# Optimization experiments

Hardware: AMD Instinct MI355X
Metric: run time of the kernel (lower is better)

## Reference

```python
import jax, jax.numpy as jnp
import numpy as np

B, N, E, F, U = 256, 240, 4338, 28, 100
NEG_SLOPE = 0.2  # PyG GATConv default negative_slope


def setup_inputs() -> dict:
    key = jax.random.key(0)
    ks = jax.random.split(key, 13)
    s = 0.05  # xavier-ish scale
    return {
        "inputs": jax.random.normal(ks[0], (B, N * F), jnp.float32),
        "state": jax.random.normal(ks[1], (B, N * U), jnp.float32),
        "edge_src": jax.random.randint(ks[2], (E,), 0, N, jnp.int32),
        "edge_dst": jax.random.randint(ks[3], (E,), 0, N, jnp.int32),
        # GATConv(U+F -> U): linear weight, attention vectors, output bias
        "Wg": jax.random.normal(ks[4], (U, U + F), jnp.float32) * s,
        "att_src": jax.random.normal(ks[5], (U,), jnp.float32) * s,
        "att_dst": jax.random.normal(ks[6], (U,), jnp.float32) * s,
        "gat_bias": jnp.zeros((U,), jnp.float32),
        # bias_1 added in _gc3 (self.biases[(100,)])
        "bias1": jnp.zeros((U,), jnp.float32),
        # GRU1: GRULinear(100, 200); GRU2: GRULinear(100, 100)
        "W_ru": jax.random.normal(ks[7], (U + F, 2 * U), jnp.float32) * s,
        "b_ru": jnp.zeros((2 * U,), jnp.float32),
        "W_c": jax.random.normal(ks[8], (U + F, U), jnp.float32) * s,
        "b_c": jnp.zeros((U,), jnp.float32),
    }


def _gat_gru(inputs, state, src, dst, Wg, att_src, att_dst, gat_bias, bias1,
             W_ru, b_ru, W_c, b_c):
    xi = inputs.reshape(B, N, F)
    xs = state.reshape(B, N, U)
    # _gc3: concat [state, inputs] -> GATConv per sample (vectorized here)
    x = jnp.concatenate([xs, xi], axis=2)                 # [B, N, U+F]
    h = jnp.einsum("bnf,cf->bnc", x, Wg)                  # [B, N, U]
    a_src = h @ att_src                                    # [B, N]
    a_dst = h @ att_dst                                    # [B, N]
    e = jax.nn.leaky_relu(a_src[:, src] + a_dst[:, dst], NEG_SLOPE)  # [B, E+N]
    eT = e.T                                               # [E+N, B]
    emax = jax.ops.segment_max(eT, dst, num_segments=N)    # [N, B]
    ex = jnp.exp(eT - emax[dst])
    denom = jax.ops.segment_sum(ex, dst, num_segments=N)   # [N, B]
    alpha = ex / denom[dst]                                # [E+N, B]
    msgs = h[:, src].transpose(1, 0, 2) * alpha[:, :, None]  # [E+N, B, U]
    agg = jax.ops.segment_sum(msgs, dst, num_segments=N)   # [N, B, U]
    gstate = agg.transpose(1, 0, 2) + gat_bias + bias1     # [B, N, U]
    st = gstate.reshape(B, N * U)
    # GRU gates (GRULinear concatenates [inputs, hidden] on feature dim)
    cat1 = jnp.concatenate([xi, gstate], axis=2).reshape(-1, U + F)
    ru = jax.nn.sigmoid((cat1 @ W_ru + b_ru).reshape(B, N, 2 * U))
    r = ru[..., :U].reshape(B, N * U)
    u = ru[..., U:].reshape(B, N * U)
    cat2 = jnp.concatenate([xi, (r * st).reshape(B, N, U)], axis=2).reshape(-1, U + F)
    c = jnp.tanh(cat2 @ W_c + b_c).reshape(B, N * U)
    return u * st + (1.0 - u) * c


def reference(inputs, state, edge_src, edge_dst, Wg, att_src, att_dst,
              gat_bias, bias1, W_ru, b_ru, W_c, b_c):
    # PyG GATConv default add_self_loops=True
    loops = jnp.arange(N, dtype=edge_src.dtype)
    src = jnp.concatenate([edge_src, loops])
    dst = jnp.concatenate([edge_dst, loops])
    return _gat_gru(inputs, state, src, dst, Wg, att_src, att_dst, gat_bias,
                    bias1, W_ru, b_ru, W_c, b_c)
```

## Files before the change

kernel.cpp:

```cpp
#include <hip/hip_runtime.h>

#define Bb 256
#define Nn 240
#define Ee 4338
#define Ff 28
#define Uu 100
#define Kk 128
#define AS 136
#define KP 248

typedef __attribute__((ext_vector_type(8))) short bf16x8;
typedef __attribute__((ext_vector_type(4))) float f32x4;
typedef unsigned short u16;

__device__ __forceinline__ float bf2f(u16 u) {
  union { unsigned int i; float f; } v; v.i = ((unsigned int)u) << 16; return v.f;
}
__device__ __forceinline__ u16 f2bf(float f) {
  union { float ff; unsigned int i; } v; v.ff = f;
  unsigned int x = v.i;
  return (u16)((x + 0x7fffu + ((x >> 16) & 1u)) >> 16);
}
__device__ __forceinline__ void split4(const float4 v, ushort4& h, ushort4& l) {
  u16 h0 = f2bf(v.x), h1 = f2bf(v.y), h2 = f2bf(v.z), h3 = f2bf(v.w);
  h.x = h0; h.y = h1; h.z = h2; h.w = h3;
  l.x = f2bf(v.x - bf2f(h0)); l.y = f2bf(v.y - bf2f(h1));
  l.z = f2bf(v.z - bf2f(h2)); l.w = f2bf(v.w - bf2f(h3));
}

__global__ __launch_bounds__(512, 2) void k_fused(
    const float* __restrict__ stt, const float* __restrict__ inp,
    const float* __restrict__ Wg,
    const float* __restrict__ att_s, const float* __restrict__ att_d,
    const int* __restrict__ esrc, const int* __restrict__ edst,
    const float* __restrict__ gbias, const float* __restrict__ b1,
    const float* __restrict__ Wru, const float* __restrict__ bru,
    const float* __restrict__ Wc, const float* __restrict__ bc,
    float* __restrict__ out) {
  __shared__ __align__(16) char smem[154752];
  u16*      hTH    = (u16*)(smem);
  u16*      hTL    = (u16*)(smem + 49600);
  u16*      panel  = (u16*)(smem + 99200);
  u16*      ahL    = panel;
  u16*      alL    = panel + 32 * AS;
  u16*      alphaL = panel;
  float*    gch    = (float*)(smem + 116608);
  u16*      panel2 = (u16*)(smem + 116608);
  u16*      alphaH = (u16*)(smem + 129408);
  u16*      ugQ    = (u16*)(smem + 145280);
  float*    asrcL  = (float*)(smem + 151680);
  float*    adstL  = (float*)(smem + 152640);
  float*    denC   = (float*)(smem + 153600);
  float*    w_asL  = (float*)(smem + 153728);
  float*    w_adL  = (float*)(smem + 154240);

  int tid = threadIdx.x;
  int b = blockIdx.x;
  const size_t sbase = (size_t)b * Nn * Uu;
  const size_t ibase = (size_t)b * Nn * Ff;

  int w = tid >> 6, l = tid & 63, l15 = l & 15, q = l >> 4;
  int cw = w * 16 + l15;

  f32x4 zero = {0.f, 0.f, 0.f, 0.f};
  bf16x8 z8 = {0, 0, 0, 0, 0, 0, 0, 0};

  auto stageChunk = [&](u16* buf, int c0, int rowsn, int base, int stride) {
    for (int j = base; j < rowsn * 32; j += stride) {
      int r = j >> 5, g = j & 31;
      float4 v = (g < 25)
          ? *(const float4*)(stt + sbase + (size_t)(c0 + r) * Uu + g * 4)
          : *(const float4*)(inp + ibase + (size_t)(c0 + r) * Ff + (g - 25) * 4);
      ushort4 hh, lo;
      split4(v, hh, lo);
      *(ushort4*)(buf + r * AS + g * 4) = hh;
      *(ushort4*)(buf + 32 * AS + r * AS + g * 4) = lo;
    }
  };

  auto histChunk = [&](int c0, int rowsn) {
    unsigned* cbase = (unsigned*)alphaH;
    for (int e = tid; e < Ee; e += 512) {
      int d = edst[e];
      unsigned r = (unsigned)(d - c0);
      if (r < (unsigned)rowsn) {
        int s = esrc[e];
        atomicAdd(&cbase[r * 124 + (s >> 1)], 1u << (16 * (s & 1)));
      }
    }
    if (tid < rowsn) {
      int n = c0 + tid;
      atomicAdd(&cbase[tid * 124 + (n >> 1)], 1u << (16 * (n & 1)));
    }
  };

  if (tid < 256) {
    int k = tid & 127;
    const float* av = (tid < 128) ? att_s : att_d;
    float acc = 0.f;
    for (int c = 0; c < Uu; ++c) acc += Wg[c * Kk + k] * av[c];
    ((tid < 128) ? w_asL : w_adL)[k] = acc;
  } else {
    stageChunk(panel, 0, 32, tid - 256, 256);
  }
  __syncthreads();

  {
    bf16x8 wh[4], wl[4];
#pragma unroll
    for (int s = 0; s < 4; ++s) {
#pragma unroll
      for (int j = 0; j < 8; ++j) {
        int kp = s * 32 + q * 8 + j;
        float v = (cw < Uu) ? Wg[cw * Kk + kp]
                : (cw == Uu) ? w_asL[kp]
                : (cw == Uu + 1) ? w_adL[kp] : 0.f;
        u16 hh = f2bf(v);
        wh[s][j] = (short)hh;
        wl[s][j] = (short)f2bf(v - bf2f(hh));
      }
    }

    for (int ch0 = 0; ch0 < Nn; ch0 += 32) {
      int rows = Nn - ch0; if (rows > 32) rows = 32;
      int nrt = rows >> 4;
      u16* bufc = ((ch0 >> 5) & 1) ? panel2 : panel;
      int nx = ch0 + 32;
      if (nx < Nn) {
        int rowsn = Nn - nx; if (rowsn > 32) rowsn = 32;
        stageChunk(((nx >> 5) & 1) ? panel2 : panel, nx, rowsn, tid, 512);
      }
      f32x4 acc[2]; acc[0] = zero; acc[1] = zero;
#pragma unroll
      for (int rt = 0; rt < 2; ++rt) if (rt < nrt) {
#pragma unroll
        for (int s = 0; s < 4; ++s) {
          bf16x8 a = *(const bf16x8*)(bufc + (rt * 16 + l15) * AS + s * 32 + q * 8);
          bf16x8 bb = *(const bf16x8*)(bufc + 32 * AS + (rt * 16 + l15) * AS + s * 32 + q * 8);
          acc[rt] = __builtin_amdgcn_mfma_f32_16x16x32_bf16(a, wh[s], acc[rt], 0, 0, 0);
          acc[rt] = __builtin_amdgcn_mfma_f32_16x16x32_bf16(bb, wh[s], acc[rt], 0, 0, 0);
          acc[rt] = __builtin_amdgcn_mfma_f32_16x16x32_bf16(a, wl[s], acc[rt], 0, 0, 0);
        }
      }
#pragma unroll
      for (int rt = 0; rt < 2; ++rt) if (rt < nrt) {
#pragma unroll
        for (int i = 0; i < 4; ++i) {
          float v = acc[rt][i];
          int krow = ch0 + rt * 16 + q * 4 + i;
          if (cw < Uu) {
            u16 hh = f2bf(v);
            hTH[cw * KP + krow] = hh;
            hTL[cw * KP + krow] = f2bf(v - bf2f(hh));
          } else if (cw == Uu) {
            asrcL[krow] = v;
          } else if (cw == Uu + 1) {
            adstL[krow] = v;
          }
        }
      }
      __syncthreads();
    }
  }

  {
    unsigned* cz = (unsigned*)alphaH;
    for (int i = tid; i < 32 * 124; i += 512) cz[i] = 0;
  }
  __syncthreads();

  histChunk(0, 32);
  bf16x8 r0h[4], r0l[4], r1h[4], r1l[4], cch[4], ccl[4];
  int cw1 = 128 + cw;
#pragma unroll
  for (int s = 0; s < 4; ++s) {
    int kb = s * 32 + q * 8;
#pragma unroll
    for (int j = 0; j < 8; ++j) {
      int kp = kb + j;
      int k = (kp < Uu) ? (kp + Ff) : (kp - Uu);
      float v0 = Wru[k * (2 * Uu) + cw];
      u16 h0 = f2bf(v0);
      r0h[s][j] = (short)h0; r0l[s][j] = (short)f2bf(v0 - bf2f(h0));
      float v1 = (cw1 < 2 * Uu) ? Wru[k * (2 * Uu) + cw1] : 0.f;
      u16 h1 = f2bf(v1);
      r1h[s][j] = (short)h1; r1l[s][j] = (short)f2bf(v1 - bf2f(h1));
      float v2 = (cw < Uu) ? Wc[k * Uu + cw] : 0.f;
      u16 h2 = f2bf(v2);
      cch[s][j] = (short)h2; ccl[s][j] = (short)f2bf(v2 - bf2f(h2));
    }
  }
  float bru0 = bru[cw];
  float bru1 = (cw1 < 2 * Uu) ? bru[cw1] : 0.f;
  float bcv = (cw < Uu) ? bc[cw] : 0.f;
  int n0 = (w >> 1) * 16 + l15;
  int n1 = (4 + (w >> 1)) * 16 + l15;
  __syncthreads();

  for (int ch0 = 0; ch0 < Nn; ch0 += 32) {
    int rows = Nn - ch0; if (rows > 32) rows = 32;
    int nrt = rows >> 4;
    int nx = ch0 + 32;
    int rows_nx = (nx < Nn) ? ((Nn - nx > 32) ? 32 : (Nn - nx)) : 0;

    {
      int d = tid >> 4, j = tid & 15;
      float dsum = 0.f;
      if (d < rows) {
        float ad = adstL[ch0 + d];
        unsigned* crow = (unsigned*)(alphaH + d * KP);
        unsigned* lrow = (unsigned*)(alphaL + d * KP);
        for (int wd = j; wd < 120; wd += 16) {
          unsigned c2 = crow[wd];
          unsigned hi2 = 0, lo2 = 0;
          if (c2) {
            unsigned ca = c2 & 0xFFFFu, cb = c2 >> 16;
            if (ca) {
              int s = 2 * wd;
              float sc = asrcL[s] + ad;
              sc = (sc > 0.f) ? sc : 0.2f * sc;
              float we = __expf(sc) * (float)ca;
              dsum += we;
              u16 hh = f2bf(we);
              hi2 |= (unsigned)hh;
              lo2 |= (unsigned)f2bf(we - bf2f(hh));
            }
            if (cb) {
              int s = 2 * wd + 1;
              float sc = asrcL[s] + ad;
              sc = (sc > 0.f) ? sc : 0.2f * sc;
              float we = __expf(sc) * (float)cb;
              dsum += we;
              u16 hh = f2bf(we);
              hi2 |= ((unsigned)hh) << 16;
              lo2 |= ((unsigned)f2bf(we - bf2f(hh))) << 16;
            }
          }
          crow[wd] = hi2;
          lrow[wd] = lo2;
        }
      }
      dsum += __shfl_xor(dsum, 1, 16);
      dsum += __shfl_xor(dsum, 2, 16);
      dsum += __shfl_xor(dsum, 4, 16);
      dsum += __shfl_xor(dsum, 8, 16);
      if (j == 0 && d < rows) denC[d] = 1.f / dsum;
    }
    __syncthreads();

#pragma unroll
    for (int p = 0; p < 2; ++p) {
      int mh = w & 1, nt = p * 4 + (w >> 1);
      if (nt > 6 || mh * 16 >= rows) continue;
      int nn = p ? n1 : n0;
      bool bv = (nn < Uu);
      int arow = (mh * 16 + l15) * KP;
      int brow = nn * KP;
      f32x4 acc = zero;
#pragma unroll
      for (int s = 0; s < 8; ++s) {
        int ko = s * 32 + q * 8;
        bool kv = (s < 7) || (q < 2);
        bf16x8 aH = kv ? *(const bf16x8*)(alphaH + arow + ko) : z8;
        bf16x8 aL = kv ? *(const bf16x8*)(alphaL + arow + ko) : z8;
        bf16x8 bH = (kv && bv) ? *(const bf16x8*)(hTH + brow + ko) : z8;
        bf16x8 bL = (kv && bv) ? *(const bf16x8*)(hTL + brow + ko) : z8;
        acc = __builtin_amdgcn_mfma_f32_16x16x32_bf16(aH, bH, acc, 0, 0, 0);
        acc = __builtin_amdgcn_mfma_f32_16x16x32_bf16(aL, bH, acc, 0, 0, 0);
        acc = __builtin_amdgcn_mfma_f32_16x16x32_bf16(aH, bL, acc, 0, 0, 0);
      }
      if (bv) {
        float gb = gbias[nn] + b1[nn];
#pragma unroll
        for (int i = 0; i < 4; ++i) {
          int m = mh * 16 + q * 4 + i;
          gch[m * Uu + nn] = acc[i] * denC[m] + gb;
        }
      }
    }
    __syncthreads();

    for (int j = tid; j < rows * 32; j += 512) {
      int r = j >> 5, g = j & 31;
      float4 v = (g < 25)
          ? *(const float4*)(gch + r * Uu + g * 4)
          : *(const float4*)(inp + ibase + (size_t)(ch0 + r) * Ff + (g - 25) * 4);
      ushort4 hh, lo;
      split4(v, hh, lo);
      *(ushort4*)(ahL + r * AS + g * 4) = hh;
      *(ushort4*)(alL + r * AS + g * 4) = lo;
    }
    if (rows_nx) {
      unsigned* cz = (unsigned*)alphaH;
      for (int i = tid; i < 32 * 124; i += 512) cz[i] = 0;
    }
    float sv[2][4];
#pragma unroll
    for (int rt = 0; rt < 2; ++rt) if (rt < nrt) {
#pragma unroll
      for (int i = 0; i < 4; ++i) {
        int row = rt * 16 + q * 4 + i;
        sv[rt][i] = (cw < Uu) ? gch[row * Uu + cw] : 0.f;
      }
    }
    __syncthreads();

    float pr[2][4];
    {
      f32x4 acc[2]; acc[0] = zero; acc[1] = zero;
#pragma unroll
      for (int rt = 0; rt < 2; ++rt) if (rt < nrt) {
#pragma unroll
        for (int s = 0; s < 4; ++s) {
          bf16x8 a = *(const bf16x8*)(ahL + (rt * 16 + l15) * AS + s * 32 + q * 8);
          bf16x8 bb = *(const bf16x8*)(alL + (rt * 16 + l15) * AS + s * 32 + q * 8);
          acc[rt] = __builtin_amdgcn_mfma_f32_16x16x32_bf16(a, r0h[s], acc[rt], 0, 0, 0);
          acc[rt] = __builtin_amdgcn_mfma_f32_16x16x32_bf16(bb, r0h[s], acc[rt], 0, 0, 0);
          acc[rt] = __builtin_amdgcn_mfma_f32_16x16x32_bf16(a, r0l[s], acc[rt], 0, 0, 0);
        }
      }
#pragma unroll
      for (int rt = 0; rt < 2; ++rt) if (rt < nrt) {
#pragma unroll
        for (int i = 0; i < 4; ++i) {
          int row = rt * 16 + q * 4 + i;
          float y = acc[rt][i] + bru0;
          float g = 1.f / (1.f + __expf(-y));
          if (cw < Uu) pr[rt][i] = g * sv[rt][i];
          else ugQ[row * Uu + (cw - Uu)] = (u16)(g * 65535.f + 0.5f);
        }
      }
    }
    {
      f32x4 acc[2]; acc[0] = zero; acc[1] = zero;
#pragma unroll
      for (int rt = 0; rt < 2; ++rt) if (rt < nrt) {
#pragma unroll
        for (int s = 0; s < 4; ++s) {
          bf16x8 a = *(const bf16x8*)(ahL + (rt * 16 + l15) * AS + s * 32 + q * 8);
          bf16x8 bb = *(const bf16x8*)(alL + (rt * 16 + l15) * AS + s * 32 + q * 8);
          acc[rt] = __builtin_amdgcn_mfma_f32_16x16x32_bf16(a, r1h[s], acc[rt], 0, 0, 0);
          acc[rt] = __builtin_amdgcn_mfma_f32_16x16x32_bf16(bb, r1h[s], acc[rt], 0, 0, 0);
          acc[rt] = __builtin_amdgcn_mfma_f32_16x16x32_bf16(a, r1l[s], acc[rt], 0, 0, 0);
        }
      }
#pragma unroll
      for (int rt = 0; rt < 2; ++rt) if (rt < nrt) {
#pragma unroll
        for (int i = 0; i < 4; ++i) {
          int row = rt * 16 + q * 4 + i;
          float y = acc[rt][i] + bru1;
          float g = 1.f / (1.f + __expf(-y));
          if (cw1 < 2 * Uu) ugQ[row * Uu + (cw1 - Uu)] = (u16)(g * 65535.f + 0.5f);
        }
      }
    }
    if (rows_nx) histChunk(nx, rows_nx);
    __syncthreads();

#pragma unroll
    for (int rt = 0; rt < 2; ++rt) if (rt < nrt) {
#pragma unroll
      for (int i = 0; i < 4; ++i) {
        int row = rt * 16 + q * 4 + i;
        if (cw < Uu) {
          float p = pr[rt][i];
          u16 hh = f2bf(p);
          ahL[row * AS + cw] = hh;
          alL[row * AS + cw] = f2bf(p - bf2f(hh));
        }
      }
    }
    __syncthreads();

    {
      f32x4 acc[2]; acc[0] = zero; acc[1] = zero;
#pragma unroll
      for (int rt = 0; rt < 2; ++rt) if (rt < nrt) {
#pragma unroll
        for (int s = 0; s < 4; ++s) {
          bf16x8 a = *(const bf16x8*)(ahL + (rt * 16 + l15) * AS + s * 32 + q * 8);
          bf16x8 bb = *(const bf16x8*)(alL + (rt * 16 + l15) * AS + s * 32 + q * 8);
          acc[rt] = __builtin_amdgcn_mfma_f32_16x16x32_bf16(a, cch[s], acc[rt], 0, 0, 0);
          acc[rt] = __builtin_amdgcn_mfma_f32_16x16x32_bf16(bb, cch[s], acc[rt], 0, 0, 0);
          acc[rt] = __builtin_amdgcn_mfma_f32_16x16x32_bf16(a, ccl[s], acc[rt], 0, 0, 0);
        }
      }
#pragma unroll
      for (int rt = 0; rt < 2; ++rt) if (rt < nrt) {
#pragma unroll
        for (int i = 0; i < 4; ++i) {
          int row = rt * 16 + q * 4 + i;
          if (cw < Uu) {
            float y = acc[rt][i] + bcv;
            float cv = 1.f - 2.f / (__expf(2.f * y) + 1.f);
            float u = (float)ugQ[row * Uu + cw] * (1.f / 65535.f);
            out[sbase + (size_t)(ch0 + row) * Uu + cw] = u * sv[rt][i] + (1.f - u) * cv;
          }
        }
      }
    }
    __syncthreads();
  }
}

extern "C" void kernel_launch(void* const* d_in, const int* in_sizes, int n_in,
                              void* d_out, int out_size, void* d_ws, size_t ws_size,
                              hipStream_t stream) {
  const float* inp   = (const float*)d_in[0];
  const float* stt   = (const float*)d_in[1];
  const int*   esrc  = (const int*)d_in[2];
  const int*   edst  = (const int*)d_in[3];
  const float* Wg    = (const float*)d_in[4];
  const float* att_s = (const float*)d_in[5];
  const float* att_d = (const float*)d_in[6];
  const float* gbias = (const float*)d_in[7];
  const float* b1    = (const float*)d_in[8];
  const float* Wru   = (const float*)d_in[9];
  const float* bru   = (const float*)d_in[10];
  const float* Wc    = (const float*)d_in[11];
  const float* bc    = (const float*)d_in[12];
  float* out = (float*)d_out;

  k_fused<<<Bb, 512, 0, stream>>>(stt, inp, Wg, att_s, att_d, esrc, edst,
                                  gbias, b1, Wru, bru, Wc, bc, out);
}
```

Before: 219.1 us.

## Split each sample across two blocks and move transposed h to global workspace

Launches two blocks per batch sample, each handling half of the destination-node chunks in the aggregation and GRU phases. The transposed hi/lo bf16 copy of h moves from LDS to a global workspace buffer, shrinking LDS from about 151KB to 54KB so more blocks can be resident per CU. Both blocks still compute the full h projection redundantly and write identical values to the same workspace region. The aggregation MFMA now reads its B operand from global/L2 instead of LDS, which adds load latency in exchange for the higher parallelism.

```diff
diff --git a/kernel.cpp b/kernel.cpp
--- a/kernel.cpp
+++ b/kernel.cpp
@@ -36,28 +36,30 @@
     const float* __restrict__ gbias, const float* __restrict__ b1,
     const float* __restrict__ Wru, const float* __restrict__ bru,
     const float* __restrict__ Wc, const float* __restrict__ bc,
+    u16* __restrict__ hTG,
     float* __restrict__ out) {
-  __shared__ __align__(16) char smem[154752];
-  u16*      hTH    = (u16*)(smem);
-  u16*      hTL    = (u16*)(smem + 49600);
-  u16*      panel  = (u16*)(smem + 99200);
+  __shared__ __align__(16) char smem[55552];
+  u16*      panel  = (u16*)(smem);
   u16*      ahL    = panel;
   u16*      alL    = panel + 32 * AS;
   u16*      alphaL = panel;
-  float*    gch    = (float*)(smem + 116608);
-  u16*      panel2 = (u16*)(smem + 116608);
-  u16*      alphaH = (u16*)(smem + 129408);
-  u16*      ugQ    = (u16*)(smem + 145280);
-  float*    asrcL  = (float*)(smem + 151680);
-  float*    adstL  = (float*)(smem + 152640);
-  float*    denC   = (float*)(smem + 153600);
-  float*    w_asL  = (float*)(smem + 153728);
-  float*    w_adL  = (float*)(smem + 154240);
+  float*    gch    = (float*)(smem + 17408);
+  u16*      panel2 = (u16*)(smem + 17408);
+  u16*      alphaH = (u16*)(smem + 30208);
+  u16*      ugQ    = (u16*)(smem + 46080);
+  float*    asrcL  = (float*)(smem + 52480);
+  float*    adstL  = (float*)(smem + 53440);
+  float*    denC   = (float*)(smem + 54400);
+  float*    w_asL  = (float*)(smem + 54528);
+  float*    w_adL  = (float*)(smem + 55040);
 
   int tid = threadIdx.x;
-  int b = blockIdx.x;
+  int b = blockIdx.x >> 1;
+  int half_blk = blockIdx.x & 1;
   const size_t sbase = (size_t)b * Nn * Uu;
   const size_t ibase = (size_t)b * Nn * Ff;
+  u16* hTHg = hTG + (size_t)b * (2 * Uu * KP);
+  u16* hTLg = hTHg + Uu * KP;
 
   int w = tid >> 6, l = tid & 63, l15 = l & 15, q = l >> 4;
   int cw = w * 16 + l15;
@@ -150,8 +152,8 @@
           int krow = ch0 + rt * 16 + q * 4 + i;
           if (cw < Uu) {
             u16 hh = f2bf(v);
-            hTH[cw * KP + krow] = hh;
-            hTL[cw * KP + krow] = f2bf(v - bf2f(hh));
+            hTHg[cw * KP + krow] = hh;
+            hTLg[cw * KP + krow] = f2bf(v - bf2f(hh));
           } else if (cw == Uu) {
             asrcL[krow] = v;
           } else if (cw == Uu + 1) {
@@ -169,7 +171,9 @@
   }
   __syncthreads();
 
-  histChunk(0, 32);
+  int chBeg = half_blk * 128;
+  int chEnd = chBeg + 128;
+  histChunk(chBeg, 32);
   bf16x8 r0h[4], r0l[4], r1h[4], r1l[4], cch[4], ccl[4];
   int cw1 = 128 + cw;
 #pragma unroll
@@ -197,11 +201,11 @@
   int n1 = (4 + (w >> 1)) * 16 + l15;
   __syncthreads();
 
-  for (int ch0 = 0; ch0 < Nn; ch0 += 32) {
+  for (int ch0 = chBeg; ch0 < chEnd && ch0 < Nn; ch0 += 32) {
     int rows = Nn - ch0; if (rows > 32) rows = 32;
     int nrt = rows >> 4;
     int nx = ch0 + 32;
-    int rows_nx = (nx < Nn) ? ((Nn - nx > 32) ? 32 : (Nn - nx)) : 0;
+    int rows_nx = (nx < chEnd && nx < Nn) ? ((Nn - nx > 32) ? 32 : (Nn - nx)) : 0;
 
     {
       int d = tid >> 4, j = tid & 15;
@@ -263,8 +267,8 @@
         bool kv = (s < 7) || (q < 2);
         bf16x8 aH = kv ? *(const bf16x8*)(alphaH + arow + ko) : z8;
         bf16x8 aL = kv ? *(const bf16x8*)(alphaL + arow + ko) : z8;
-        bf16x8 bH = (kv && bv) ? *(const bf16x8*)(hTH + brow + ko) : z8;
-        bf16x8 bL = (kv && bv) ? *(const bf16x8*)(hTL + brow + ko) : z8;
+        bf16x8 bH = (kv && bv) ? *(const bf16x8*)(hTHg + brow + ko) : z8;
+        bf16x8 bL = (kv && bv) ? *(const bf16x8*)(hTLg + brow + ko) : z8;
         acc = __builtin_amdgcn_mfma_f32_16x16x32_bf16(aH, bH, acc, 0, 0, 0);
         acc = __builtin_amdgcn_mfma_f32_16x16x32_bf16(aL, bH, acc, 0, 0, 0);
         acc = __builtin_amdgcn_mfma_f32_16x16x32_bf16(aH, bL, acc, 0, 0, 0);
@@ -421,7 +425,8 @@
   const float* Wc    = (const float*)d_in[11];
   const float* bc    = (const float*)d_in[12];
   float* out = (float*)d_out;
-
-  k_fused<<<Bb, 512, 0, stream>>>(stt, inp, Wg, att_s, att_d, esrc, edst,
-                                  gbias, b1, Wru, bru, Wc, bc, out);
+  u16* hTG = (u16*)d_ws;
+
+  k_fused<<<Bb * 2, 512, 0, stream>>>(stt, inp, Wg, att_s, att_d, esrc, edst,
+                                      gbias, b1, Wru, bru, Wc, bc, hTG, out);
 }
```

Result: slower. 302.3 us (+38.0%).
